# Optimization experiments

Hardware: AMD Instinct MI355X
Metric: run time of the kernel (lower is better)

The kernel has to match this reference:

```python
import jax, jax.numpy as jnp
import numpy as np

OUT, IN = 4096, 4096      # self.shape
DENSITY = 0.01
BATCH, SEQ = 4, 2048


def setup_inputs() -> dict:
    key = jax.random.key(0)
    k_x, k_v = jax.random.split(key)
    nnz = int(DENSITY * OUT * IN)
    # Build a valid CSR structure (static metadata, like set_mask()).
    rng = np.random.default_rng(0)
    base = nnz // OUT
    counts = np.full(OUT, base, dtype=np.int64)
    counts[: nnz - base * OUT] += 1
    row_offs = np.zeros(OUT + 1, dtype=np.int32)
    row_offs[1:] = np.cumsum(counts)
    col_idx = np.sort(rng.integers(0, IN, size=nnz)).astype(np.int32)
    # re-sort columns within each row for canonical CSR
    col_idx = np.concatenate([np.sort(rng.integers(0, IN, size=c)) for c in counts]).astype(np.int32)
    x = jax.random.normal(k_x, (BATCH, SEQ, IN), dtype=jnp.float32)
    values = jax.random.normal(k_v, (nnz,), dtype=jnp.float32) * 0.02
    return {
        "x": x,
        "values": values,
        "row_offs": jnp.asarray(row_offs),
        "col_idx": jnp.asarray(col_idx),
    }


def reference(x, values, row_offs, col_idx):
    # y = x @ W^T where W is CSR(values, row_offs, col_idx) of shape (OUT, IN).
    rows = row_offs.shape[0] - 1
    nnz = values.shape[0]
    counts = jnp.diff(row_offs)
    # row id of every nonzero (CSR expansion); total_repeat_length keeps it jit-able
    row_ids = jnp.repeat(jnp.arange(rows, dtype=jnp.int32), counts,
                         total_repeat_length=nnz)
    # scratch is the efficient XLA form of SpMM (same math as spops CSR kernel).
    W = jnp.zeros((rows, x.shape[-1]), dtype=values.dtype).at[row_ids, col_idx].add(values)
    return jnp.einsum("bsi,oi->bso", x, W)
```

## Files before the change

### kernel.cpp

```cpp
#include <hip/hip_runtime.h>
#include <hip/hip_fp16.h>
#include <stdint.h>

#define IN_DIM   4096
#define OUT_DIM  4096
#define TPB      512
#define TOKS     8

typedef float  f32x4 __attribute__((ext_vector_type(4)));

__device__ __forceinline__ uint32_t pack_f16x2(float a, float b) {
    auto h = __builtin_amdgcn_cvt_pkrtz(a, b);
    uint32_t u;
    __builtin_memcpy(&u, &h, 4);
    return u;
}

__device__ __forceinline__ void stage_x_tile(const float* __restrict__ x,
                                             size_t tb, uint32_t* xs, int tid) {
    const int lane = tid & 63;
    const int wave = tid >> 6;
    const int tp   = lane >> 4;
    const int rot  = (lane >> 1) & 3;
    const float* xa = x + (tb + 2 * (size_t)tp) * IN_DIM;
    const float* xb = xa + IN_DIM;
    #pragma unroll
    for (int it = 0; it < IN_DIM / 4 / 128; ++it) {
        const int c4 = (lane & 15) + 16 * wave + 128 * it;
        const f32x4 a = __builtin_nontemporal_load(
            reinterpret_cast<const f32x4*>(xa + 4 * c4));
        const f32x4 b = __builtin_nontemporal_load(
            reinterpret_cast<const f32x4*>(xb + 4 * c4));
        const uint32_t d0 = pack_f16x2(a[0], b[0]);
        const uint32_t d1 = pack_f16x2(a[1], b[1]);
        const uint32_t d2 = pack_f16x2(a[2], b[2]);
        const uint32_t d3 = pack_f16x2(a[3], b[3]);
        const uint32_t t0 = (rot & 2) ? d2 : d0;
        const uint32_t t1 = (rot & 2) ? d3 : d1;
        const uint32_t t2 = (rot & 2) ? d0 : d2;
        const uint32_t t3 = (rot & 2) ? d1 : d3;
        const uint32_t u0 = (rot & 1) ? t1 : t0;
        const uint32_t u1 = (rot & 1) ? t2 : t1;
        const uint32_t u2 = (rot & 1) ? t3 : t2;
        const uint32_t u3 = (rot & 1) ? t0 : t3;
        const int cb = 4 * c4;
        xs[(cb + ((0 + rot) & 3)) * 4 + tp] = u0;
        xs[(cb + ((1 + rot) & 3)) * 4 + tp] = u1;
        xs[(cb + ((2 + rot) & 3)) * 4 + tp] = u2;
        xs[(cb + ((3 + rot) & 3)) * 4 + tp] = u3;
    }
}

__global__ void build_ell(const float* __restrict__ values,
                          const int* __restrict__ row_offs,
                          const int* __restrict__ col_idx,
                          uint4* __restrict__ ell4, int galloc) {
    const int idx = blockIdx.x * blockDim.x + threadIdx.x;
    const int r = idx & (OUT_DIM - 1);
    const int g = idx >> 12;
    if (g >= galloc) return;
    const int beg = row_offs[r];
    const int end = row_offs[r + 1];
    uint32_t e0 = 0, e1 = 0, e2 = 0, e3 = 0;
    #pragma unroll
    for (int j = 0; j < 4; ++j) {
        const int k = 4 * g + j;
        uint32_t u = 0;
        if (beg + k < end) {
            const uint32_t c = (uint32_t)col_idx[beg + k];
            uint32_t vb = __float_as_uint(values[beg + k]);
            vb = (vb + 0x7fffu + ((vb >> 16) & 1u)) & 0xffff0000u;
            u = vb | (c << 4);
        }
        if (j == 0) e0 = u; else if (j == 1) e1 = u; else if (j == 2) e2 = u; else e3 = u;
    }
    ell4[(size_t)g * OUT_DIM + r] = make_uint4(e0, e1, e2, e3);
}

#define FMA8(E, D)                                                   \
    do {                                                             \
        const float v_ = __uint_as_float(E);                         \
        const __half2* h_ = reinterpret_cast<const __half2*>(&(D));  \
        acc0 = fmaf(__low2float(h_[0]),  v_, acc0);                  \
        acc1 = fmaf(__high2float(h_[0]), v_, acc1);                  \
        acc2 = fmaf(__low2float(h_[1]),  v_, acc2);                  \
        acc3 = fmaf(__high2float(h_[1]), v_, acc3);                  \
        acc4 = fmaf(__low2float(h_[2]),  v_, acc4);                  \
        acc5 = fmaf(__high2float(h_[2]), v_, acc5);                  \
        acc6 = fmaf(__low2float(h_[3]),  v_, acc6);                  \
        acc7 = fmaf(__high2float(h_[3]), v_, acc7);                  \
    } while (0)

#define GATH(D, E)                                                           \
    (D) = *reinterpret_cast<const uint4*>(reinterpret_cast<const char*>(xs) + \
                                          ((E) & 0xfff0u))

__global__ __launch_bounds__(TPB, 4)
void spmm_ell(const float* __restrict__ x, const uint4* __restrict__ ell4,
              float* __restrict__ y, int ng) {
    __shared__ __align__(16) uint32_t xs[IN_DIM * (TOKS / 2)];
    const int tid  = threadIdx.x;
    const size_t tb = (size_t)blockIdx.x * TOKS;

    stage_x_tile(x, tb, xs, tid);
    __syncthreads();

    #pragma unroll 1
    for (int chunk = 0; chunk < OUT_DIM / TPB; ++chunk) {
        const int r = chunk * TPB + tid;
        float acc0 = 0.f, acc1 = 0.f, acc2 = 0.f, acc3 = 0.f;
        float acc4 = 0.f, acc5 = 0.f, acc6 = 0.f, acc7 = 0.f;
        const uint4* ep = ell4 + r;

        uint4 eA = ep[0];
        uint4 dA0, dA1, dA2, dA3;
        GATH(dA0, eA.x); GATH(dA1, eA.y); GATH(dA2, eA.z); GATH(dA3, eA.w);
        uint4 eB = ep[OUT_DIM];
        uint4 dB0, dB1, dB2, dB3;
        const uint4* epn = ep + 2 * (size_t)OUT_DIM;

        #pragma unroll 1
        for (int g = 0; g + 2 < ng; g += 2) {
            const uint4 tA = epn[0];
            GATH(dB0, eB.x); GATH(dB1, eB.y); GATH(dB2, eB.z); GATH(dB3, eB.w);
            FMA8(eA.x, dA0); FMA8(eA.y, dA1); FMA8(eA.z, dA2); FMA8(eA.w, dA3);
            const uint4 tB = epn[OUT_DIM];
            GATH(dA0, tA.x); GATH(dA1, tA.y); GATH(dA2, tA.z); GATH(dA3, tA.w);
            FMA8(eB.x, dB0); FMA8(eB.y, dB1); FMA8(eB.z, dB2); FMA8(eB.w, dB3);
            eA = tA; eB = tB;
            epn += 2 * (size_t)OUT_DIM;
        }
        FMA8(eA.x, dA0); FMA8(eA.y, dA1); FMA8(eA.z, dA2); FMA8(eA.w, dA3);

        __builtin_nontemporal_store(acc0, &y[(tb + 0) * OUT_DIM + r]);
        __builtin_nontemporal_store(acc1, &y[(tb + 1) * OUT_DIM + r]);
        __builtin_nontemporal_store(acc2, &y[(tb + 2) * OUT_DIM + r]);
        __builtin_nontemporal_store(acc3, &y[(tb + 3) * OUT_DIM + r]);
        __builtin_nontemporal_store(acc4, &y[(tb + 4) * OUT_DIM + r]);
        __builtin_nontemporal_store(acc5, &y[(tb + 5) * OUT_DIM + r]);
        __builtin_nontemporal_store(acc6, &y[(tb + 6) * OUT_DIM + r]);
        __builtin_nontemporal_store(acc7, &y[(tb + 7) * OUT_DIM + r]);
    }
}

__global__ __launch_bounds__(TPB, 4)
void spmm_csr(const float* __restrict__ x, const float* __restrict__ values,
              const int* __restrict__ row_offs, const int* __restrict__ col_idx,
              float* __restrict__ y) {
    __shared__ __align__(16) uint32_t xs[IN_DIM * (TOKS / 2)];
    const int tid  = threadIdx.x;
    const size_t tb = (size_t)blockIdx.x * TOKS;

    stage_x_tile(x, tb, xs, tid);
    __syncthreads();

    #pragma unroll 1
    for (int chunk = 0; chunk < OUT_DIM / TPB; ++chunk) {
        const int r = chunk * TPB + tid;
        float acc0 = 0.f, acc1 = 0.f, acc2 = 0.f, acc3 = 0.f;
        float acc4 = 0.f, acc5 = 0.f, acc6 = 0.f, acc7 = 0.f;
        int k = row_offs[r];
        const int ke = row_offs[r + 1];
        for (; k < ke; ++k) {
            const uint32_t e = __float_as_uint(values[k]);
            const uint32_t off = (uint32_t)col_idx[k] << 4;
            uint4 d;
            GATH(d, off);
            FMA8(e, d);
        }
        y[(tb + 0) * OUT_DIM + r] = acc0;
        y[(tb + 1) * OUT_DIM + r] = acc1;
        y[(tb + 2) * OUT_DIM + r] = acc2;
        y[(tb + 3) * OUT_DIM + r] = acc3;
        y[(tb + 4) * OUT_DIM + r] = acc4;
        y[(tb + 5) * OUT_DIM + r] = acc5;
        y[(tb + 6) * OUT_DIM + r] = acc6;
        y[(tb + 7) * OUT_DIM + r] = acc7;
    }
}

extern "C" void kernel_launch(void* const* d_in, const int* in_sizes, int n_in,
                              void* d_out, int out_size, void* d_ws, size_t ws_size,
                              hipStream_t stream) {
    const float* x        = (const float*)d_in[0];
    const float* values   = (const float*)d_in[1];
    const int*   row_offs = (const int*)d_in[2];
    const int*   col_idx  = (const int*)d_in[3];
    float* y = (float*)d_out;

    const int nnz  = in_sizes[1];
    const int rows = in_sizes[2] - 1;
    const int ntok = in_sizes[0] / IN_DIM;
    const int kmax = nnz / rows + ((nnz % rows) ? 1 : 0);

    int ng = (kmax + 3) / 4;
    if (!(ng & 1)) ++ng;
    const int galloc = ng + 1;

    dim3 grid(ntok / TOKS), block(TPB);
    const size_t ell_bytes = (size_t)galloc * OUT_DIM * sizeof(uint4);
    if (ws_size >= ell_bytes) {
        uint4* ell4 = (uint4*)d_ws;
        const int nthr = OUT_DIM * galloc;
        build_ell<<<dim3((nthr + 255) / 256), dim3(256), 0, stream>>>(
            values, row_offs, col_idx, ell4, galloc);
        spmm_ell<<<grid, block, 0, stream>>>(x, ell4, y, ng);
    } else {
        spmm_csr<<<grid, block, 0, stream>>>(x, values, row_offs, col_idx, y);
    }
}
```

Measured before the change: 112.2 us.

## Reorder ELL nonzeros per slot to spread LDS bank accesses

```diff
diff --git a/kernel.cpp b/kernel.cpp
--- a/kernel.cpp
+++ b/kernel.cpp
@@ -55,26 +55,45 @@
                           const int* __restrict__ row_offs,
                           const int* __restrict__ col_idx,
                           uint4* __restrict__ ell4, int galloc) {
-    const int idx = blockIdx.x * blockDim.x + threadIdx.x;
-    const int r = idx & (OUT_DIM - 1);
-    const int g = idx >> 12;
-    if (g >= galloc) return;
+    const int r = blockIdx.x * blockDim.x + threadIdx.x;
+    if (r >= OUT_DIM) return;
     const int beg = row_offs[r];
     const int end = row_offs[r + 1];
-    uint32_t e0 = 0, e1 = 0, e2 = 0, e3 = 0;
-    #pragma unroll
-    for (int j = 0; j < 4; ++j) {
-        const int k = 4 * g + j;
-        uint32_t u = 0;
-        if (beg + k < end) {
-            const uint32_t c = (uint32_t)col_idx[beg + k];
-            uint32_t vb = __float_as_uint(values[beg + k]);
-            vb = (vb + 0x7fffu + ((vb >> 16) & 1u)) & 0xffff0000u;
-            u = vb | (c << 4);
+    int klen = end - beg;
+    const int nslot = 4 * galloc;
+    if (klen > nslot) klen = nslot;
+    const bool reorder = (klen <= 64);
+    uint64_t used = 0;
+
+    for (int g = 0; g < galloc; ++g) {
+        uint32_t e0 = 0, e1 = 0, e2 = 0, e3 = 0;
+        #pragma unroll
+        for (int j4 = 0; j4 < 4; ++j4) {
+            const int j = 4 * g + j4;
+            uint32_t u = 0;
+            if (j < klen) {
+                int pick = j;
+                if (reorder) {
+                    const int t = (j + r) & 7;
+                    int best = -1, bestd = 9;
+                    for (int i = 0; i < klen; ++i) {
+                        if ((used >> i) & 1ull) continue;
+                        const int d = ((col_idx[beg + i] & 7) - t) & 7;
+                        if (d < bestd) { bestd = d; best = i; if (d == 0) break; }
+                    }
+                    used |= 1ull << best;
+                    pick = best;
+                }
+                const uint32_t c = (uint32_t)col_idx[beg + pick];
+                uint32_t vb = __float_as_uint(values[beg + pick]);
+                vb = (vb + 0x7fffu + ((vb >> 16) & 1u)) & 0xffff0000u;
+                u = vb | (c << 4);
+            }
+            if (j4 == 0) e0 = u; else if (j4 == 1) e1 = u;
+            else if (j4 == 2) e2 = u; else e3 = u;
         }
-        if (j == 0) e0 = u; else if (j == 1) e1 = u; else if (j == 2) e2 = u; else e3 = u;
-    }
-    ell4[(size_t)g * OUT_DIM + r] = make_uint4(e0, e1, e2, e3);
+        ell4[(size_t)g * OUT_DIM + r] = make_uint4(e0, e1, e2, e3);
+    }
 }
 
 #define FMA8(E, D)                                                   \
@@ -201,8 +220,7 @@
     const size_t ell_bytes = (size_t)galloc * OUT_DIM * sizeof(uint4);
     if (ws_size >= ell_bytes) {
         uint4* ell4 = (uint4*)d_ws;
-        const int nthr = OUT_DIM * galloc;
-        build_ell<<<dim3((nthr + 255) / 256), dim3(256), 0, stream>>>(
+        build_ell<<<dim3((OUT_DIM + 255) / 256), dim3(256), 0, stream>>>(
             values, row_offs, col_idx, ell4, galloc);
         spmm_ell<<<grid, block, 0, stream>>>(x, ell4, y, ng);
     } else {
```

Result: slower. 403.2 us (+259.2%).
